# Kernel tuning notes

Hardware: AMD Instinct MI355X
Metric: run time of the kernel (lower is better)

The kernel has to match this reference:

```python
import jax, jax.numpy as jnp
import numpy as np

B, L, C, H, S = 32, 4096, 512, 8, 8
NW = L // S          # slide_num = 512 windows
D = C // H           # head dim = 64


def setup_inputs() -> dict:
    key = jax.random.key(0)
    ks = jax.random.split(key, 6)
    p = lambda k, sh: jax.random.normal(k, sh, jnp.float32) * 0.02
    return {
        'x': jax.random.normal(ks[0], (B, L, C), jnp.float32),
        'Wq': p(ks[1], (C, C)), 'bq': jnp.zeros((C,), jnp.float32),
        'Wk': p(ks[2], (C, C)), 'bk': jnp.zeros((C,), jnp.float32),
        'Wv': p(ks[3], (C, C)), 'bv': jnp.zeros((C,), jnp.float32),
        'Wp': p(ks[4], (C, C)), 'bp': jnp.zeros((C,), jnp.float32),
        'bias_table': p(ks[5], (2 * S - 1, H)),  # trunc_normal(std=0.02) analogue
    }


def _shift_mask():
    # Swin-style shift mask: segment ids 0 / 1 / 2 over the last window's halves.
    seg = np.zeros(L, np.float32)
    seg[L - S:L - S // 2] = 1.0
    seg[L - S // 2:] = 2.0
    mw = seg.reshape(NW, S)                       # [NW, S]
    diff = mw[:, :, None] - mw[:, None, :]        # [NW, S, S]
    return jnp.asarray(np.where(diff != 0, -100.0, 0.0), jnp.float32)


def reference(x, Wq, bq, Wk, bk, Wv, bv, Wp, bp, bias_table):
    # shift=True: roll left by S//2, window, attend, unwindow, roll back
    xs = jnp.roll(x, -S // 2, axis=1).reshape(B * NW, S, C)

    def heads(w, b):
        return (xs @ w + b).reshape(B * NW, S, H, D).transpose(0, 2, 1, 3)

    q, k, v = heads(Wq, bq), heads(Wk, bk), heads(Wv, bv)
    # NOTE: original scales by sqrt(emb_size), not sqrt(head_dim)
    energy = jnp.einsum('bhqd,bhkd->bhqk', q, k) / jnp.sqrt(jnp.float32(C))

    # relative position bias: index[i, j] = j - i + S - 1
    idx = jnp.arange(S)[None, :] - jnp.arange(S)[:, None] + (S - 1)
    bias = bias_table[idx].transpose(2, 0, 1)     # [H, S, S]
    energy = energy + bias[None]

    mask = _shift_mask()                          # [NW, S, S]
    energy = energy.reshape(B, NW, H, S, S) + mask[None, :, None]
    att = jax.nn.softmax(energy, axis=-1).reshape(B * NW, H, S, S)

    out = jnp.einsum('bhqk,bhkd->bhqd', att, v)
    out = out.transpose(0, 2, 1, 3).reshape(B * NW, S, C)
    out = out @ Wp + bp
    return jnp.roll(out.reshape(B, L, C), S // 2, axis=1)
```

## Files before the change

kernel.cpp:

```cpp
#include <hip/hip_runtime.h>
#include <stdint.h>
#include <type_traits>


typedef unsigned short ushort_t;
typedef __bf16 v8bf __attribute__((ext_vector_type(8)));
typedef float v4f __attribute__((ext_vector_type(4)));

__device__ __forceinline__ ushort_t f2bf(float f) {
  unsigned int u = __float_as_uint(f);
  u = u + 0x7fffu + ((u >> 16) & 1u);
  return (ushort_t)(u >> 16);
}

__global__ __launch_bounds__(256) void prep_kernel(
    const float* __restrict__ Wq, const float* __restrict__ Wk,
    const float* __restrict__ Wv, const float* __restrict__ Wp,
    const float* __restrict__ bq, const float* __restrict__ bk,
    const float* __restrict__ bv,
    ushort_t* __restrict__ WTqkv, ushort_t* __restrict__ WTp,
    float* __restrict__ bqkvf)
{
  int idx = blockIdx.x * 256 + threadIdx.x;
  if (idx < 786432) {
    int n = idx % 1536;
    int k = idx / 1536;
    const float* W = (n < 512) ? Wq : (n < 1024) ? Wk : Wv;
    WTqkv[(size_t)n * 512 + k] = f2bf(W[k * 512 + (n & 511)]);
  } else if (idx < 1048576) {
    int j = idx - 786432;
    int n = j & 511;
    int k = j >> 9;
    WTp[(size_t)n * 512 + k] = f2bf(Wp[k * 512 + n]);
  } else if (idx < 1050112) {
    int n = idx - 1048576;
    const float* bb = (n < 512) ? bq : (n < 1024) ? bk : bv;
    bqkvf[n] = bb[n & 511];
  }
}

__global__ __launch_bounds__(256) void convert_roll_kernel(
    const float* __restrict__ x, ushort_t* __restrict__ xb)
{
  const int t = blockIdx.x * 256 + threadIdx.x;
  const int m = t >> 6;
  const int ch = t & 63;
  const int b = m >> 12;
  const int r = m & 4095;
  const int src = (b << 12) | ((r + 4) & 4095);
  const float4* p = (const float4*)(x + (size_t)src * 512 + ch * 8);
  float4 a0 = p[0], a1 = p[1];
  uint4 o;
  o.x = (unsigned)f2bf(a0.x) | ((unsigned)f2bf(a0.y) << 16);
  o.y = (unsigned)f2bf(a0.z) | ((unsigned)f2bf(a0.w) << 16);
  o.z = (unsigned)f2bf(a1.x) | ((unsigned)f2bf(a1.y) << 16);
  o.w = (unsigned)f2bf(a1.z) | ((unsigned)f2bf(a1.w) << 16);
  *(uint4*)(xb + (size_t)m * 512 + ch * 8) = o;
}

template<int LDC, int NT, bool ROLL_C, typename OutT>
__global__ __launch_bounds__(256) void gemm_bt(
    const ushort_t* __restrict__ A, const ushort_t* __restrict__ BT,
    const float* __restrict__ bias, OutT* __restrict__ C)
{
  __shared__ __align__(16) ushort_t As[128 * 64];
  __shared__ __align__(16) ushort_t Bs[128 * 64];

  const int tid = threadIdx.x;
  const int l   = tid & 63;
  const int wv  = tid >> 6;
  const int wm  = wv >> 1;
  const int wn  = wv & 1;

  const int m0    = blockIdx.y * 128;
  const int nbase = blockIdx.x * (NT * 128);

  const int skcol   = (l & 7) * 8;
  const int lds_off = wv * 512 + l * 8;
  const int fr = l & 15;
  const int fq = l >> 4;

  for (int nt = 0; nt < NT; ++nt) {
    const int n0 = nbase + nt * 128;
    v4f acc[4][4];
#pragma unroll
    for (int i = 0; i < 4; ++i)
#pragma unroll
      for (int j = 0; j < 4; ++j) acc[i][j] = (v4f){0.f, 0.f, 0.f, 0.f};

    for (int kt = 0; kt < 8; ++kt) {
      const int k0 = kt * 64;
      __syncthreads();
#pragma unroll
      for (int p = 0; p < 4; ++p) {
        const int gm = m0 + p * 32 + wv * 8 + (l >> 3);
        const ushort_t* ap = A + (size_t)gm * 512 + k0 + skcol;
        __builtin_amdgcn_global_load_lds(
            (const __attribute__((address_space(1))) void*)ap,
            (__attribute__((address_space(3))) void*)(As + p * 2048 + lds_off),
            16, 0, 0);
        const int gn = n0 + p * 32 + wv * 8 + (l >> 3);
        const ushort_t* bp = BT + (size_t)gn * 512 + k0 + skcol;
        __builtin_amdgcn_global_load_lds(
            (const __attribute__((address_space(1))) void*)bp,
            (__attribute__((address_space(3))) void*)(Bs + p * 2048 + lds_off),
            16, 0, 0);
      }
      __syncthreads();
#pragma unroll
      for (int kk = 0; kk < 2; ++kk) {
        const int ko = kk * 32 + fq * 8;
        v8bf af[4], bf[4];
#pragma unroll
        for (int mi = 0; mi < 4; ++mi)
          af[mi] = *(const v8bf*)(As + (wm * 64 + mi * 16 + fr) * 64 + ko);
#pragma unroll
        for (int ni = 0; ni < 4; ++ni)
          bf[ni] = *(const v8bf*)(Bs + (wn * 64 + ni * 16 + fr) * 64 + ko);
#pragma unroll
        for (int mi = 0; mi < 4; ++mi)
#pragma unroll
          for (int ni = 0; ni < 4; ++ni)
            acc[mi][ni] = __builtin_amdgcn_mfma_f32_16x16x32_bf16(
                af[mi], bf[ni], acc[mi][ni], 0, 0, 0);
      }
    }

#pragma unroll
    for (int mi = 0; mi < 4; ++mi) {
#pragma unroll
      for (int ni = 0; ni < 4; ++ni) {
        const int col = n0 + wn * 64 + ni * 16 + fr;
        const float bv = bias[col];
#pragma unroll
        for (int r = 0; r < 4; ++r) {
          int row = m0 + wm * 64 + mi * 16 + fq * 4 + r;
          if (ROLL_C) row = (row & ~4095) | ((row + 4) & 4095);
          const float val = acc[mi][ni][r] + bv;
          if constexpr (std::is_same_v<OutT, float>) {
            C[(size_t)row * LDC + col] = val;
          } else {
            C[(size_t)row * LDC + col] = f2bf(val);
          }
        }
      }
    }
  }
}

__device__ __forceinline__ void unpack8(uint4 v, float* f) {
  f[0] = __uint_as_float(v.x << 16); f[1] = __uint_as_float(v.x & 0xffff0000u);
  f[2] = __uint_as_float(v.y << 16); f[3] = __uint_as_float(v.y & 0xffff0000u);
  f[4] = __uint_as_float(v.z << 16); f[5] = __uint_as_float(v.z & 0xffff0000u);
  f[6] = __uint_as_float(v.w << 16); f[7] = __uint_as_float(v.w & 0xffff0000u);
}

__global__ __launch_bounds__(256) void attn_kernel(
    const ushort_t* __restrict__ qkv, const float* __restrict__ bias_table,
    ushort_t* __restrict__ attout)
{
  __shared__ float btab[120];
  if (threadIdx.x < 120) btab[threadIdx.x] = bias_table[threadIdx.x];
  __syncthreads();

  const int l  = threadIdx.x & 63;
  const int wv = threadIdx.x >> 6;
  const int u  = blockIdx.x * 4 + wv;
  const int b  = u >> 12;
  const int w  = (u >> 3) & 511;
  const int h  = u & 7;
  const int i  = l >> 3;
  const int c  = l & 7;

  const size_t rowi = (size_t)(b << 12) + (w << 3) + i;
  const ushort_t* pq = qkv + rowi * 1536 + h * 64 + c * 8;
  uint4 q8 = *(const uint4*)pq;
  uint4 k8 = *(const uint4*)(pq + 512);
  uint4 v8 = *(const uint4*)(pq + 1024);

  float qf[8];
  unpack8(q8, qf);

  float e[8];
#pragma unroll
  for (int t = 0; t < 8; ++t) {
    const int src = (l + 8 * t) & 63;
    uint4 kc;
    kc.x = __shfl((int)k8.x, src); kc.y = __shfl((int)k8.y, src);
    kc.z = __shfl((int)k8.z, src); kc.w = __shfl((int)k8.w, src);
    float kf[8]; unpack8(kc, kf);
    float s = 0.f;
#pragma unroll
    for (int d = 0; d < 8; ++d) s = fmaf(qf[d], kf[d], s);
    s += __shfl_xor(s, 1);
    s += __shfl_xor(s, 2);
    s += __shfl_xor(s, 4);
    e[t] = s;
  }

  const float scale = 0.044194173824159216f;
#pragma unroll
  for (int t = 0; t < 8; ++t) {
    const int j = (i + t) & 7;
    float ev = e[t] * scale + btab[(j - i + 7) * 8 + h];
    if (w == 511 && ((i < 4) != (j < 4))) ev -= 100.f;
    e[t] = ev;
  }

  float mx = e[0];
#pragma unroll
  for (int t = 1; t < 8; ++t) mx = fmaxf(mx, e[t]);
  float p[8], sum = 0.f;
#pragma unroll
  for (int t = 0; t < 8; ++t) { p[t] = __expf(e[t] - mx); sum += p[t]; }
  const float inv = __fdividef(1.f, sum);

  float of[8] = {0.f, 0.f, 0.f, 0.f, 0.f, 0.f, 0.f, 0.f};
#pragma unroll
  for (int t = 0; t < 8; ++t) {
    const int src = (l + 8 * t) & 63;
    uint4 vc;
    vc.x = __shfl((int)v8.x, src); vc.y = __shfl((int)v8.y, src);
    vc.z = __shfl((int)v8.z, src); vc.w = __shfl((int)v8.w, src);
    float vf[8]; unpack8(vc, vf);
    const float a = p[t] * inv;
#pragma unroll
    for (int d = 0; d < 8; ++d) of[d] = fmaf(a, vf[d], of[d]);
  }

  uint4 o;
  o.x = (unsigned)f2bf(of[0]) | ((unsigned)f2bf(of[1]) << 16);
  o.y = (unsigned)f2bf(of[2]) | ((unsigned)f2bf(of[3]) << 16);
  o.z = (unsigned)f2bf(of[4]) | ((unsigned)f2bf(of[5]) << 16);
  o.w = (unsigned)f2bf(of[6]) | ((unsigned)f2bf(of[7]) << 16);
  *(uint4*)(attout + rowi * 512 + h * 64 + c * 8) = o;
}

extern "C" void kernel_launch(void* const* d_in, const int* in_sizes, int n_in,
                              void* d_out, int out_size, void* d_ws, size_t ws_size,
                              hipStream_t stream) {
  (void)in_sizes; (void)n_in; (void)out_size; (void)ws_size;
  const float* x  = (const float*)d_in[0];
  const float* Wq = (const float*)d_in[1];
  const float* bq = (const float*)d_in[2];
  const float* Wk = (const float*)d_in[3];
  const float* bk = (const float*)d_in[4];
  const float* Wv = (const float*)d_in[5];
  const float* bv = (const float*)d_in[6];
  const float* Wp = (const float*)d_in[7];
  const float* bp = (const float*)d_in[8];
  const float* bt = (const float*)d_in[9];

  char* ws = (char*)d_ws;
  ushort_t* qkv    = (ushort_t*)(ws);
  ushort_t* xb     = (ushort_t*)(ws + 402653184ull);
  ushort_t* attout = xb;
  ushort_t* WTqkv  = (ushort_t*)(ws + 536870912ull);
  ushort_t* WTp    = (ushort_t*)(ws + 538443776ull);
  float*    bqkvf  = (float*)  (ws + 538968064ull);

  prep_kernel<<<4103, 256, 0, stream>>>(Wq, Wk, Wv, Wp, bq, bk, bv,
                                        WTqkv, WTp, bqkvf);
  convert_roll_kernel<<<32768, 256, 0, stream>>>(x, xb);
  gemm_bt<1536, 4, false, ushort_t><<<dim3(3, 1024), 256, 0, stream>>>(
      xb, WTqkv, bqkvf, qkv);
  attn_kernel<<<32768, 256, 0, stream>>>(qkv, bt, attout);
  gemm_bt<512, 2, true, float><<<dim3(2, 1024), 256, 0, stream>>>(
      attout, WTp, bp, (float*)d_out);
}
```

Measured before the change: 1.075 ms.

## Replace 128x128 GEMM with pipelined 256x256 tile, 8 waves, swizzled LDS

```diff
diff --git a/kernel.cpp b/kernel.cpp
--- a/kernel.cpp
+++ b/kernel.cpp
@@ -58,94 +58,179 @@
   *(uint4*)(xb + (size_t)m * 512 + ch * 8) = o;
 }
 
-template<int LDC, int NT, bool ROLL_C, typename OutT>
-__global__ __launch_bounds__(256) void gemm_bt(
+
+#define SB() __builtin_amdgcn_sched_barrier(0)
+
+__device__ __forceinline__ void stage_half(
+    const ushort_t* __restrict__ G, ushort_t* lds_b, int boff,
+    int kt, int half, int rowbase, int tid)
+{
+  ushort_t* Lb = lds_b + boff + (((kt & 1) << 1) + half) * 8192;
+  const int rb = rowbase + (half << 7);
+#pragma unroll
+  for (int i = 0; i < 2; ++i) {
+    const int c = tid + (i << 9);
+    const int row = c >> 3;
+    const int slot = c & 7;
+    const int scol = (slot ^ (row & 7)) << 3;
+    const ushort_t* src = G + (size_t)(rb + row) * 512 + (kt << 6) + scol;
+    __builtin_amdgcn_global_load_lds(
+        (const __attribute__((address_space(1))) void*)src,
+        (__attribute__((address_space(3))) void*)(Lb + ((size_t)c << 3)),
+        16, 0, 0);
+  }
+}
+
+__device__ __forceinline__ void mfma_quad(
+    v4f (&accq)[2][4], const v8bf (&af)[2][2], const v8bf (&bq)[4][2])
+{
+#pragma unroll
+  for (int mi = 0; mi < 2; ++mi)
+#pragma unroll
+    for (int ni = 0; ni < 4; ++ni)
+#pragma unroll
+      for (int kk = 0; kk < 2; ++kk)
+        accq[mi][ni] = __builtin_amdgcn_mfma_f32_16x16x32_bf16(
+            af[mi][kk], bq[ni][kk], accq[mi][ni], 0, 0, 0);
+}
+
+template<int LDC, int GN, bool ROLL_C, typename OutT>
+__global__ __launch_bounds__(512, 2) void gemm256(
     const ushort_t* __restrict__ A, const ushort_t* __restrict__ BT,
     const float* __restrict__ bias, OutT* __restrict__ C)
 {
-  __shared__ __align__(16) ushort_t As[128 * 64];
-  __shared__ __align__(16) ushort_t Bs[128 * 64];
+  extern __shared__ ushort_t lds[];
 
   const int tid = threadIdx.x;
   const int l   = tid & 63;
   const int wv  = tid >> 6;
-  const int wm  = wv >> 1;
-  const int wn  = wv & 1;
-
-  const int m0    = blockIdx.y * 128;
-  const int nbase = blockIdx.x * (NT * 128);
-
-  const int skcol   = (l & 7) * 8;
-  const int lds_off = wv * 512 + l * 8;
-  const int fr = l & 15;
-  const int fq = l >> 4;
-
-  for (int nt = 0; nt < NT; ++nt) {
-    const int n0 = nbase + nt * 128;
-    v4f acc[4][4];
-#pragma unroll
-    for (int i = 0; i < 4; ++i)
-#pragma unroll
-      for (int j = 0; j < 4; ++j) acc[i][j] = (v4f){0.f, 0.f, 0.f, 0.f};
-
-    for (int kt = 0; kt < 8; ++kt) {
-      const int k0 = kt * 64;
-      __syncthreads();
-#pragma unroll
-      for (int p = 0; p < 4; ++p) {
-        const int gm = m0 + p * 32 + wv * 8 + (l >> 3);
-        const ushort_t* ap = A + (size_t)gm * 512 + k0 + skcol;
-        __builtin_amdgcn_global_load_lds(
-            (const __attribute__((address_space(1))) void*)ap,
-            (__attribute__((address_space(3))) void*)(As + p * 2048 + lds_off),
-            16, 0, 0);
-        const int gn = n0 + p * 32 + wv * 8 + (l >> 3);
-        const ushort_t* bp = BT + (size_t)gn * 512 + k0 + skcol;
-        __builtin_amdgcn_global_load_lds(
-            (const __attribute__((address_space(1))) void*)bp,
-            (__attribute__((address_space(3))) void*)(Bs + p * 2048 + lds_off),
-            16, 0, 0);
-      }
-      __syncthreads();
-#pragma unroll
-      for (int kk = 0; kk < 2; ++kk) {
-        const int ko = kk * 32 + fq * 8;
-        v8bf af[4], bf[4];
-#pragma unroll
-        for (int mi = 0; mi < 4; ++mi)
-          af[mi] = *(const v8bf*)(As + (wm * 64 + mi * 16 + fr) * 64 + ko);
-#pragma unroll
-        for (int ni = 0; ni < 4; ++ni)
-          bf[ni] = *(const v8bf*)(Bs + (wn * 64 + ni * 16 + fr) * 64 + ko);
-#pragma unroll
-        for (int mi = 0; mi < 4; ++mi)
-#pragma unroll
-          for (int ni = 0; ni < 4; ++ni)
-            acc[mi][ni] = __builtin_amdgcn_mfma_f32_16x16x32_bf16(
-                af[mi], bf[ni], acc[mi][ni], 0, 0, 0);
-      }
-    }
-
-#pragma unroll
-    for (int mi = 0; mi < 4; ++mi) {
-#pragma unroll
-      for (int ni = 0; ni < 4; ++ni) {
-        const int col = n0 + wn * 64 + ni * 16 + fr;
-        const float bv = bias[col];
-#pragma unroll
-        for (int r = 0; r < 4; ++r) {
-          int row = m0 + wm * 64 + mi * 16 + fq * 4 + r;
-          if (ROLL_C) row = (row & ~4095) | ((row + 4) & 4095);
-          const float val = acc[mi][ni][r] + bv;
-          if constexpr (std::is_same_v<OutT, float>) {
-            C[(size_t)row * LDC + col] = val;
-          } else {
-            C[(size_t)row * LDC + col] = f2bf(val);
+  const int wr  = wv >> 1;
+  const int wc  = wv & 1;
+  const int fr  = l & 15;
+  const int fq  = l >> 4;
+
+  constexpr int NWG = GN * 512;
+  const int bid = blockIdx.x;
+  const int swz = (bid & 7) * (NWG >> 3) + (bid >> 3);
+  const int m0 = (swz / GN) * 256;
+  const int n0 = (swz % GN) * 256;
+
+  const int arow = wr * 32 + fr;
+  const int brow = wc * 64 + fr;
+  const int kswz = (fr & 7) << 3;
+  const int kb   = fq << 3;
+
+#define LDA_FRAGS(bufq) do { \
+  _Pragma("unroll") for (int mi = 0; mi < 2; ++mi) \
+  _Pragma("unroll") for (int kk = 0; kk < 2; ++kk) \
+    af[mi][kk] = *(const v8bf*)(lds + (bufq) * 8192 + \
+        (arow + mi * 16) * 64 + ((kk * 32 + kb) ^ kswz)); \
+} while (0)
+#define LDB_FRAGS(qn, bufq) do { \
+  _Pragma("unroll") for (int ni = 0; ni < 4; ++ni) \
+  _Pragma("unroll") for (int kk = 0; kk < 2; ++kk) \
+    bfr[qn][ni][kk] = *(const v8bf*)(lds + 32768 + (bufq) * 8192 + \
+        (brow + ni * 16) * 64 + ((kk * 32 + kb) ^ kswz)); \
+} while (0)
+#define MFMA_PHASE(QM, QN) do { \
+  SB(); __builtin_amdgcn_s_barrier(); SB(); \
+  __builtin_amdgcn_s_setprio(1); \
+  mfma_quad(acc[QM][QN], af, bfr[QN]); \
+  __builtin_amdgcn_s_setprio(0); \
+  SB(); } while (0)
+#define ENDBAR() do { __builtin_amdgcn_s_barrier(); SB(); } while (0)
+
+  v4f acc[2][2][2][4];
+#pragma unroll
+  for (int a = 0; a < 2; ++a)
+#pragma unroll
+    for (int b = 0; b < 2; ++b)
+#pragma unroll
+      for (int m = 0; m < 2; ++m)
+#pragma unroll
+        for (int n = 0; n < 4; ++n)
+          acc[a][b][m][n] = (v4f){0.f, 0.f, 0.f, 0.f};
+
+  stage_half(A,  lds, 0,     0, 0, m0, tid);
+  stage_half(BT, lds, 32768, 0, 0, n0, tid);
+  stage_half(A,  lds, 0,     0, 1, m0, tid);
+  stage_half(BT, lds, 32768, 0, 1, n0, tid);
+  stage_half(A,  lds, 0,     1, 0, m0, tid);
+  stage_half(BT, lds, 32768, 1, 0, n0, tid);
+  SB();
+  asm volatile("s_waitcnt vmcnt(4)" ::: "memory");
+  __builtin_amdgcn_s_barrier();
+  SB();
+
+  for (int t = 0; t < 4; ++t) {
+    const bool more = (t < 3);
+    const int o = 2 * t + 1;
+    v8bf af[2][2];
+    v8bf bfr[2][4][2];
+
+    LDA_FRAGS(0);
+    LDB_FRAGS(0, 0);
+    stage_half(A, lds, 0, o, 1, m0, tid);
+    MFMA_PHASE(0, 0);
+    ENDBAR();
+    LDB_FRAGS(1, 1);
+    stage_half(BT, lds, 32768, o, 1, n0, tid);
+    MFMA_PHASE(0, 1);
+    ENDBAR();
+    LDA_FRAGS(1);
+    if (more) stage_half(A, lds, 0, o + 1, 0, m0, tid);
+    MFMA_PHASE(1, 0);
+    ENDBAR();
+    if (more) stage_half(BT, lds, 32768, o + 1, 0, n0, tid);
+    MFMA_PHASE(1, 1);
+    if (t == 3) asm volatile("s_waitcnt vmcnt(0)" ::: "memory");
+    else        asm volatile("s_waitcnt vmcnt(4)" ::: "memory");
+    ENDBAR();
+    LDA_FRAGS(2);
+    LDB_FRAGS(0, 2);
+    if (more) stage_half(A, lds, 0, o + 1, 1, m0, tid);
+    MFMA_PHASE(0, 0);
+    ENDBAR();
+    LDB_FRAGS(1, 3);
+    if (more) stage_half(BT, lds, 32768, o + 1, 1, n0, tid);
+    MFMA_PHASE(0, 1);
+    ENDBAR();
+    LDA_FRAGS(3);
+    if (more) stage_half(A, lds, 0, o + 2, 0, m0, tid);
+    MFMA_PHASE(1, 0);
+    ENDBAR();
+    if (more) stage_half(BT, lds, 32768, o + 2, 0, n0, tid);
+    MFMA_PHASE(1, 1);
+    asm volatile("s_waitcnt vmcnt(4)" ::: "memory");
+    ENDBAR();
+  }
+
+#pragma unroll
+  for (int Qm = 0; Qm < 2; ++Qm)
+#pragma unroll
+    for (int Qn = 0; Qn < 2; ++Qn)
+#pragma unroll
+      for (int mi = 0; mi < 2; ++mi)
+#pragma unroll
+        for (int ni = 0; ni < 4; ++ni) {
+          const int col = n0 + Qn * 128 + wc * 64 + ni * 16 + fr;
+          const float bv = bias[col];
+#pragma unroll
+          for (int r = 0; r < 4; ++r) {
+            int row = m0 + Qm * 128 + wr * 32 + mi * 16 + fq * 4 + r;
+            if (ROLL_C) row = (row & ~4095) | ((row + 4) & 4095);
+            const float val = acc[Qm][Qn][mi][ni][r] + bv;
+            if constexpr (std::is_same_v<OutT, float>)
+              C[(size_t)row * LDC + col] = val;
+            else
+              C[(size_t)row * LDC + col] = f2bf(val);
           }
         }
-      }
-    }
-  }
+
+#undef LDA_FRAGS
+#undef LDB_FRAGS
+#undef MFMA_PHASE
+#undef ENDBAR
 }
 
 __device__ __forceinline__ void unpack8(uint4 v, float* f) {
@@ -262,9 +347,9 @@
   prep_kernel<<<4103, 256, 0, stream>>>(Wq, Wk, Wv, Wp, bq, bk, bv,
                                         WTqkv, WTp, bqkvf);
   convert_roll_kernel<<<32768, 256, 0, stream>>>(x, xb);
-  gemm_bt<1536, 4, false, ushort_t><<<dim3(3, 1024), 256, 0, stream>>>(
+  gemm256<1536, 6, false, ushort_t><<<3072, 512, 131072, stream>>>(
       xb, WTqkv, bqkvf, qkv);
   attn_kernel<<<32768, 256, 0, stream>>>(qkv, bt, attout);
-  gemm_bt<512, 2, true, float><<<dim3(2, 1024), 256, 0, stream>>>(
+  gemm256<512, 2, true, float><<<1024, 512, 131072, stream>>>(
       attout, WTp, bp, (float*)d_out);
 }
```

Result: faster. 1.046 ms (-2.7%).
